# Kernel optimization log

Measured on AMD Instinct MI355X. Metric: run time of the kernel, lower is better.

The kernel has to match this reference:

```python
import jax, jax.numpy as jnp
import numpy as np

TWO_PI = 2.0 * np.pi
LN_EPS = 1e-5


def _periods(out_dim, nb):
    # periods[i,j,g] = i*(out_dim*nb) + j*nb + g + 2
    return jnp.arange(out_dim * out_dim * nb, dtype=jnp.float32).reshape(out_dim, out_dim, nb) + 2.0


def _layer(x, M, gamma, beta, P, residual):
    # x: (B,S,in), M: (out,in), P: (out,out,nb)
    out_dim, _, nb = P.shape
    S = x.shape[1]
    xt = jnp.matmul(x, M.T)  # (B,S,out)
    mu = jnp.mean(xt, axis=-1, keepdims=True)
    var = jnp.mean((xt - mu) ** 2, axis=-1, keepdims=True)
    xn = (xt - mu) / jnp.sqrt(var + LN_EPS) * gamma + beta
    pos = jnp.arange(S, dtype=jnp.float32)[:, None, None, None]  # (S,1,1,1)
    phi = jnp.cos(TWO_PI * pos / _periods(out_dim, nb)[None])  # (S,out,out,nb)
    W = jnp.einsum('ijg,sijg->sij', P, phi)  # (S,out,out) contract basis first
    Nk = jnp.einsum('bsj,sij->bsi', xn, W)  # (B,S,out)
    return Nk + residual


def setup_inputs() -> dict:
    key = jax.random.key(0)
    ks = jax.random.split(key, 8)
    B, S, D_in, D, NB = 8, 1024, 64, 96, 8
    u = lambda k, shape, a: jax.random.uniform(k, shape, jnp.float32, -a, a)
    return {
        'seq': jax.random.normal(ks[0], (B, S, D_in), jnp.float32),
        'M1': u(ks[1], (D, D_in), 0.5),
        'P1': u(ks[2], (D, D, NB), 0.1),
        'Wres1': u(ks[3], (D, D_in), 0.1),
        'g1': jnp.ones((D,), jnp.float32),
        'b1': jnp.zeros((D,), jnp.float32),
        'M2': u(ks[4], (D, D), 0.5),
        'P2': u(ks[5], (D, D, NB), 0.1),
        'g2': jnp.ones((D,), jnp.float32),
        'b2': jnp.zeros((D,), jnp.float32),
    }


def reference(seq, M1, P1, Wres1, g1, b1, M2, P2, g2, b2):
    # Layer 1: 64 -> 96, 'separate' residual uses a Linear projection
    x1 = _layer(seq, M1, g1, b1, P1, jnp.matmul(seq, Wres1.T))
    # Layer 2: 96 -> 96, 'separate' residual with in_dim==out_dim is Identity
    x2 = _layer(x1, M2, g2, b2, P2, x1)
    return x2
```

## Files before the change

kernel.cpp:

```cpp
#include <hip/hip_runtime.h>
#include <hip/hip_fp16.h>

#define S_LEN    1024
#define B_SZ     8
#define D_IN     64
#define D_OUT    96
#define NB       8
#define NE       (D_OUT * D_OUT)
#define CHUNK    16
#define NCHUNK   (S_LEN / CHUNK)
#define NT_W     256
#define NWBLK    (NCHUNK * (NE / NT_W))
#define NT_C     512
#define HPAD     104
#define SPAD     100
#define XPAD     68

__device__ __forceinline__ float cos_rev(float v) {
    v -= floorf(v);
    return __builtin_amdgcn_cosf(v);
}

__global__ void __launch_bounds__(NT_W)
w_kernel(const float* __restrict__ P1, const float* __restrict__ P2,
         __half* __restrict__ W1, __half* __restrict__ W2) {
    const int c  = blockIdx.x / (NE / NT_W);
    const int eb = blockIdx.x % (NE / NT_W);
    const int e  = eb * NT_W + threadIdx.x;
    const int s0 = c * CHUNK;
    const float s0f = (float)s0;

    float p1l[NB], p2l[NB];
    *(float4*)&p1l[0] = *(const float4*)(P1 + e * NB);
    *(float4*)&p1l[4] = *(const float4*)(P1 + e * NB + 4);
    *(float4*)&p2l[0] = *(const float4*)(P2 + e * NB);
    *(float4*)&p2l[4] = *(const float4*)(P2 + e * NB + 4);

    float cc[NB], cp[NB], kk[NB];
    #pragma unroll
    for (int g = 0; g < NB; ++g) {
        const float inv = __builtin_amdgcn_rcpf((float)(e * NB + 2 + g));
        cc[g] = cos_rev(s0f * inv);
        cp[g] = cos_rev((s0f - 1.0f) * inv);
        kk[g] = 2.0f * __builtin_amdgcn_cosf(inv);
    }

    #pragma unroll 4
    for (int s = s0; s < s0 + CHUNK; ++s) {
        float a1 = 0.0f, a2 = 0.0f;
        #pragma unroll
        for (int g = 0; g < NB; ++g) {
            a1 = fmaf(p1l[g], cc[g], a1);
            a2 = fmaf(p2l[g], cc[g], a2);
        }
        W1[s * NE + e] = __float2half(a1);
        W2[s * NE + e] = __float2half(a2);
        #pragma unroll
        for (int g = 0; g < NB; ++g) {
            float cn = fmaf(kk[g], cc[g], -cp[g]);
            cp[g] = cc[g];
            cc[g] = cn;
        }
    }
}

__device__ __forceinline__ float nkdot(const __half* __restrict__ wrow,
                                       const float* __restrict__ xr) {
    float acc = 0.0f;
    #pragma unroll
    for (int h = 0; h < 2; ++h) {
        #pragma unroll
        for (int j = h * 6; j < h * 6 + 6; ++j) {
            float4 raw = *(const float4*)(wrow + 8 * j);
            const __half2* hp = (const __half2*)&raw;
            float2 c0 = __half22float2(hp[0]);
            float2 c1 = __half22float2(hp[1]);
            float2 c2 = __half22float2(hp[2]);
            float2 c3 = __half22float2(hp[3]);
            float4 x0 = *(const float4*)(xr + 8 * j);
            float4 x1 = *(const float4*)(xr + 8 * j + 4);
            acc = fmaf(c0.x, x0.x, acc); acc = fmaf(c0.y, x0.y, acc);
            acc = fmaf(c1.x, x0.z, acc); acc = fmaf(c1.y, x0.w, acc);
            acc = fmaf(c2.x, x1.x, acc); acc = fmaf(c2.y, x1.y, acc);
            acc = fmaf(c3.x, x1.z, acc); acc = fmaf(c3.y, x1.w, acc);
        }
    }
    return acc;
}

__device__ __forceinline__ void stage_W(__half* __restrict__ wh,
                                        const __half* __restrict__ Wg,
                                        int tid) {
    for (int cidx = tid; cidx < NE / 8; cidx += NT_C) {
        const int i = cidx / 12;
        const int j = (cidx % 12) * 8;
        *(float4*)(wh + i * HPAD + j) = *(const float4*)(Wg + cidx * 8);
    }
}

__global__ void __launch_bounds__(NT_C)
consumer(const float* __restrict__ seq,
         const float* __restrict__ M1, const float* __restrict__ Wres1,
         const float* __restrict__ M2,
         const float* __restrict__ g1, const float* __restrict__ b1,
         const float* __restrict__ g2, const float* __restrict__ b2,
         const __half* __restrict__ W1g, const __half* __restrict__ W2g,
         float* __restrict__ out) {
    __shared__ __align__(16) __half wh [D_OUT * HPAD];
    __shared__ __align__(16) float  xn [B_SZ * SPAD];
    __shared__ __align__(16) float  x1b[B_SZ * SPAD];

    const int s   = blockIdx.x;
    const int tid = threadIdx.x;

    stage_W(wh, W1g + (size_t)s * NE, tid);
    {
        int b = tid >> 6, k = tid & 63;
        x1b[b * SPAD + k] = seq[((size_t)b * S_LEN + s) * D_IN + k];
    }
    __syncthreads();

    float ar0 = 0.0f, ar1 = 0.0f;
    for (int pass = 0; pass < 2; ++pass) {
        int idx = tid + pass * NT_C;
        if (idx >= B_SZ * D_OUT) break;
        int i = idx >> 3, b = idx & 7;
        const float4* m  = (const float4*)(M1 + i * D_IN);
        const float4* wr = (const float4*)(Wres1 + i * D_IN);
        const float*  xr = x1b + b * SPAD;
        float at = 0.0f, ar = 0.0f;
        #pragma unroll
        for (int k = 0; k < D_IN / 4; ++k) {
            float4 mv = m[k], rv = wr[k];
            float x0 = xr[4*k], x1 = xr[4*k+1], x2 = xr[4*k+2], x3 = xr[4*k+3];
            at = fmaf(mv.x, x0, fmaf(mv.y, x1, fmaf(mv.z, x2, fmaf(mv.w, x3, at))));
            ar = fmaf(rv.x, x0, fmaf(rv.y, x1, fmaf(rv.z, x2, fmaf(rv.w, x3, ar))));
        }
        xn[b * SPAD + i] = at;
        if (pass == 0) ar0 = ar; else ar1 = ar;
    }
    __syncthreads();

    {
        const int b = tid >> 6, lane = tid & 63;
        const bool lo = (lane < 32);
        float* row = xn + b * SPAD;
        float v0 = row[lane];
        float v1 = lo ? row[64 + lane] : 0.0f;
        float sum = v0 + v1, sq = fmaf(v0, v0, v1 * v1);
        #pragma unroll
        for (int off = 32; off > 0; off >>= 1) {
            sum += __shfl_down(sum, off, 64);
            sq  += __shfl_down(sq,  off, 64);
        }
        sum = __shfl(sum, 0, 64);
        sq  = __shfl(sq,  0, 64);
        const float mu  = sum * (1.0f / 96.0f);
        const float var = fmaf(sq, 1.0f / 96.0f, -(mu * mu));
        const float rs  = rsqrtf(var + 1e-5f);
        row[lane] = fmaf((v0 - mu) * rs, g1[lane], b1[lane]);
        if (lo) row[64 + lane] = fmaf((v1 - mu) * rs, g1[64 + lane], b1[64 + lane]);
    }
    __syncthreads();

    for (int pass = 0; pass < 2; ++pass) {
        int idx = tid + pass * NT_C;
        if (idx >= B_SZ * D_OUT) break;
        int i = idx >> 3, b = idx & 7;
        float ar = (pass == 0) ? ar0 : ar1;
        x1b[b * SPAD + i] = ar + nkdot(wh + i * HPAD, xn + b * SPAD);
    }
    __syncthreads();

    stage_W(wh, W2g + (size_t)s * NE, tid);

    for (int pass = 0; pass < 2; ++pass) {
        int idx = tid + pass * NT_C;
        if (idx >= B_SZ * D_OUT) break;
        int i = idx >> 3, b = idx & 7;
        const float4* m  = (const float4*)(M2 + i * D_OUT);
        const float*  xr = x1b + b * SPAD;
        float at = 0.0f;
        #pragma unroll
        for (int k = 0; k < D_OUT / 4; ++k) {
            float4 mv = m[k];
            at = fmaf(mv.x, xr[4*k], fmaf(mv.y, xr[4*k+1],
                 fmaf(mv.z, xr[4*k+2], fmaf(mv.w, xr[4*k+3], at))));
        }
        xn[b * SPAD + i] = at;
    }
    __syncthreads();

    {
        const int b = tid >> 6, lane = tid & 63;
        const bool lo = (lane < 32);
        float* row = xn + b * SPAD;
        float v0 = row[lane];
        float v1 = lo ? row[64 + lane] : 0.0f;
        float sum = v0 + v1, sq = fmaf(v0, v0, v1 * v1);
        #pragma unroll
        for (int off = 32; off > 0; off >>= 1) {
            sum += __shfl_down(sum, off, 64);
            sq  += __shfl_down(sq,  off, 64);
        }
        sum = __shfl(sum, 0, 64);
        sq  = __shfl(sq,  0, 64);
        const float mu  = sum * (1.0f / 96.0f);
        const float var = fmaf(sq, 1.0f / 96.0f, -(mu * mu));
        const float rs  = rsqrtf(var + 1e-5f);
        row[lane] = fmaf((v0 - mu) * rs, g2[lane], b2[lane]);
        if (lo) row[64 + lane] = fmaf((v1 - mu) * rs, g2[64 + lane], b2[64 + lane]);
    }
    __syncthreads();

    for (int pass = 0; pass < 2; ++pass) {
        int idx = tid + pass * NT_C;
        if (idx >= B_SZ * D_OUT) break;
        int i = idx >> 3, b = idx & 7;
        float acc = nkdot(wh + i * HPAD, xn + b * SPAD);
        out[((size_t)b * S_LEN + s) * D_OUT + i] = acc + x1b[b * SPAD + i];
    }
}

__global__ void __launch_bounds__(NT_W)
hier_fallback(const float* __restrict__ seq,  const float* __restrict__ M1,
              const float* __restrict__ P1,   const float* __restrict__ Wres1,
              const float* __restrict__ g1,   const float* __restrict__ b1,
              const float* __restrict__ M2,   const float* __restrict__ P2,
              const float* __restrict__ g2,   const float* __restrict__ b2,
              float* __restrict__ out) {
    __shared__ __align__(16) float w[D_OUT * SPAD];
    __shared__ __align__(16) float xin[B_SZ * XPAD];
    __shared__ __align__(16) float xn [B_SZ * SPAD];
    __shared__ __align__(16) float x1b[B_SZ * SPAD];
    const int s = blockIdx.x, tid = threadIdx.x;
    const float sf = (float)s;

    for (int idx = tid; idx < B_SZ * D_IN; idx += NT_W) {
        int b = idx >> 6, k = idx & (D_IN - 1);
        xin[b * XPAD + k] = seq[(b * S_LEN + s) * D_IN + k];
    }
    for (int e = tid; e < NE; e += NT_W) {
        float pl[8];
        *(float4*)&pl[0] = *(const float4*)(P1 + e * NB);
        *(float4*)&pl[4] = *(const float4*)(P1 + e * NB + 4);
        float acc = 0.0f;
        #pragma unroll
        for (int g = 0; g < NB; ++g) {
            float v = sf * __builtin_amdgcn_rcpf((float)(e * NB + 2 + g));
            acc = fmaf(pl[g], cos_rev(v), acc);
        }
        int i = e / D_OUT;
        w[e + (SPAD - D_OUT) * i] = acc;
    }
    __syncthreads();
    for (int idx = tid; idx < B_SZ * D_OUT; idx += NT_W) {
        int i = idx >> 3, b = idx & 7;
        const float4* m  = (const float4*)(M1 + i * D_IN);
        const float4* wr = (const float4*)(Wres1 + i * D_IN);
        const float*  xr = xin + b * XPAD;
        float at = 0.0f, ar = 0.0f;
        #pragma unroll
        for (int k = 0; k < D_IN / 4; ++k) {
            float4 mv = m[k], rv = wr[k];
            float x0 = xr[4*k], x1 = xr[4*k+1], x2 = xr[4*k+2], x3 = xr[4*k+3];
            at = fmaf(mv.x, x0, fmaf(mv.y, x1, fmaf(mv.z, x2, fmaf(mv.w, x3, at))));
            ar = fmaf(rv.x, x0, fmaf(rv.y, x1, fmaf(rv.z, x2, fmaf(rv.w, x3, ar))));
        }
        xn [b * SPAD + i] = at;
        x1b[b * SPAD + i] = ar;
    }
    __syncthreads();
    {
        const int b = tid >> 5, rr = tid & 31;
        float* row = xn + b * SPAD;
        float v0 = row[rr], v1 = row[rr + 32], v2 = row[rr + 64];
        float sum = v0 + v1 + v2, sq = fmaf(v0, v0, fmaf(v1, v1, v2 * v2));
        #pragma unroll
        for (int off = 16; off > 0; off >>= 1) {
            sum += __shfl_down(sum, off, 32);
            sq  += __shfl_down(sq,  off, 32);
        }
        sum = __shfl(sum, 0, 32); sq = __shfl(sq, 0, 32);
        float mu = sum * (1.0f/96.0f), var = fmaf(sq, 1.0f/96.0f, -(mu*mu));
        float rs = rsqrtf(var + 1e-5f);
        row[rr]      = fmaf((v0 - mu) * rs, g1[rr],      b1[rr]);
        row[rr + 32] = fmaf((v1 - mu) * rs, g1[rr + 32], b1[rr + 32]);
        row[rr + 64] = fmaf((v2 - mu) * rs, g1[rr + 64], b1[rr + 64]);
    }
    __syncthreads();
    for (int idx = tid; idx < B_SZ * D_OUT; idx += NT_W) {
        int i = idx >> 3, b = idx & 7;
        const float* wrow = w + i * SPAD;
        const float* xr   = xn + b * SPAD;
        float acc = 0.0f;
        #pragma unroll
        for (int j = 0; j < D_OUT / 4; ++j) {
            float4 wv = *(const float4*)(wrow + 4 * j);
            float4 xv = *(const float4*)(xr + 4 * j);
            acc = fmaf(wv.x, xv.x, fmaf(wv.y, xv.y, fmaf(wv.z, xv.z, fmaf(wv.w, xv.w, acc))));
        }
        x1b[b * SPAD + i] += acc;
    }
    __syncthreads();
    for (int e = tid; e < NE; e += NT_W) {
        float pl[8];
        *(float4*)&pl[0] = *(const float4*)(P2 + e * NB);
        *(float4*)&pl[4] = *(const float4*)(P2 + e * NB + 4);
        float acc = 0.0f;
        #pragma unroll
        for (int g = 0; g < NB; ++g) {
            float v = sf * __builtin_amdgcn_rcpf((float)(e * NB + 2 + g));
            acc = fmaf(pl[g], cos_rev(v), acc);
        }
        int i = e / D_OUT;
        w[e + (SPAD - D_OUT) * i] = acc;
    }
    for (int idx = tid; idx < B_SZ * D_OUT; idx += NT_W) {
        int i = idx >> 3, b = idx & 7;
        const float4* m  = (const float4*)(M2 + i * D_OUT);
        const float*  xr = x1b + b * SPAD;
        float at = 0.0f;
        #pragma unroll
        for (int k = 0; k < D_OUT / 4; ++k) {
            float4 mv = m[k];
            at = fmaf(mv.x, xr[4*k], fmaf(mv.y, xr[4*k+1],
                 fmaf(mv.z, xr[4*k+2], fmaf(mv.w, xr[4*k+3], at))));
        }
        xn[b * SPAD + i] = at;
    }
    __syncthreads();
    {
        const int b = tid >> 5, rr = tid & 31;
        float* row = xn + b * SPAD;
        float v0 = row[rr], v1 = row[rr + 32], v2 = row[rr + 64];
        float sum = v0 + v1 + v2, sq = fmaf(v0, v0, fmaf(v1, v1, v2 * v2));
        #pragma unroll
        for (int off = 16; off > 0; off >>= 1) {
            sum += __shfl_down(sum, off, 32);
            sq  += __shfl_down(sq,  off, 32);
        }
        sum = __shfl(sum, 0, 32); sq = __shfl(sq, 0, 32);
        float mu = sum * (1.0f/96.0f), var = fmaf(sq, 1.0f/96.0f, -(mu*mu));
        float rs = rsqrtf(var + 1e-5f);
        row[rr]      = fmaf((v0 - mu) * rs, g2[rr],      b2[rr]);
        row[rr + 32] = fmaf((v1 - mu) * rs, g2[rr + 32], b2[rr + 32]);
        row[rr + 64] = fmaf((v2 - mu) * rs, g2[rr + 64], b2[rr + 64]);
    }
    __syncthreads();
    for (int idx = tid; idx < B_SZ * D_OUT; idx += NT_W) {
        int i = idx >> 3, b = idx & 7;
        const float* wrow = w + i * SPAD;
        const float* xr   = xn + b * SPAD;
        float acc = 0.0f;
        #pragma unroll
        for (int j = 0; j < D_OUT / 4; ++j) {
            float4 wv = *(const float4*)(wrow + 4 * j);
            float4 xv = *(const float4*)(xr + 4 * j);
            acc = fmaf(wv.x, xv.x, fmaf(wv.y, xv.y, fmaf(wv.z, xv.z, fmaf(wv.w, xv.w, acc))));
        }
        out[(b * S_LEN + s) * D_OUT + i] = acc + x1b[b * SPAD + i];
    }
}

extern "C" void kernel_launch(void* const* d_in, const int* in_sizes, int n_in,
                              void* d_out, int out_size, void* d_ws, size_t ws_size,
                              hipStream_t stream) {
    const float* seq   = (const float*)d_in[0];
    const float* M1    = (const float*)d_in[1];
    const float* P1    = (const float*)d_in[2];
    const float* Wres1 = (const float*)d_in[3];
    const float* g1    = (const float*)d_in[4];
    const float* b1    = (const float*)d_in[5];
    const float* M2    = (const float*)d_in[6];
    const float* P2    = (const float*)d_in[7];
    const float* g2    = (const float*)d_in[8];
    const float* b2    = (const float*)d_in[9];
    float* out = (float*)d_out;

    const size_t need = (size_t)2 * S_LEN * NE * sizeof(__half);
    if (ws_size >= need) {
        __half* W1 = (__half*)d_ws;
        __half* W2 = W1 + (size_t)S_LEN * NE;
        w_kernel<<<dim3(NWBLK), dim3(NT_W), 0, stream>>>(P1, P2, W1, W2);
        consumer<<<dim3(S_LEN), dim3(NT_C), 0, stream>>>(
            seq, M1, Wres1, M2, g1, b1, g2, b2, W1, W2, out);
    } else {
        hier_fallback<<<dim3(S_LEN), dim3(NT_W), 0, stream>>>(
            seq, M1, P1, Wres1, g1, b1, M2, P2, g2, b2, out);
    }
}
```

Before: 120.4 us.

## Fuse projection matmul with LayerNorm per wavefront and enlarge W chunk size

The consumer kernel now gives each wavefront one batch row. It computes the input projection and residual for that row directly in registers and reduces mean and variance with shuffles, so the intermediate shared-memory round trip and one barrier per layer go away. The residual is stored into x1b and the Nk dot product is accumulated into it in place. The W-generation chunk size is doubled, which halves the number of w_kernel blocks and changes per-block work. Projection work is now uneven, with half the lanes doing two rows, and M1/M2 rows are read with a lane-strided pattern that may coalesce less well.

```diff
diff --git a/kernel.cpp b/kernel.cpp
--- a/kernel.cpp
+++ b/kernel.cpp
@@ -7,7 +7,7 @@
 #define D_OUT    96
 #define NB       8
 #define NE       (D_OUT * D_OUT)
-#define CHUNK    16
+#define CHUNK    32
 #define NCHUNK   (S_LEN / CHUNK)
 #define NT_W     256
 #define NWBLK    (NCHUNK * (NE / NT_W))
@@ -110,44 +110,47 @@
     __shared__ __align__(16) float  xn [B_SZ * SPAD];
     __shared__ __align__(16) float  x1b[B_SZ * SPAD];
 
-    const int s   = blockIdx.x;
-    const int tid = threadIdx.x;
+    const int s    = blockIdx.x;
+    const int tid  = threadIdx.x;
+    const int wv   = tid >> 6;
+    const int lane = tid & 63;
+
+    {
+        x1b[wv * SPAD + lane] = seq[((size_t)wv * S_LEN + s) * D_IN + lane];
+    }
+    __syncthreads();
 
     stage_W(wh, W1g + (size_t)s * NE, tid);
+
     {
-        int b = tid >> 6, k = tid & 63;
-        x1b[b * SPAD + k] = seq[((size_t)b * S_LEN + s) * D_IN + k];
-    }
-    __syncthreads();
-
-    float ar0 = 0.0f, ar1 = 0.0f;
-    for (int pass = 0; pass < 2; ++pass) {
-        int idx = tid + pass * NT_C;
-        if (idx >= B_SZ * D_OUT) break;
-        int i = idx >> 3, b = idx & 7;
-        const float4* m  = (const float4*)(M1 + i * D_IN);
-        const float4* wr = (const float4*)(Wres1 + i * D_IN);
-        const float*  xr = x1b + b * SPAD;
-        float at = 0.0f, ar = 0.0f;
-        #pragma unroll
-        for (int k = 0; k < D_IN / 4; ++k) {
-            float4 mv = m[k], rv = wr[k];
-            float x0 = xr[4*k], x1 = xr[4*k+1], x2 = xr[4*k+2], x3 = xr[4*k+3];
-            at = fmaf(mv.x, x0, fmaf(mv.y, x1, fmaf(mv.z, x2, fmaf(mv.w, x3, at))));
-            ar = fmaf(rv.x, x0, fmaf(rv.y, x1, fmaf(rv.z, x2, fmaf(rv.w, x3, ar))));
-        }
-        xn[b * SPAD + i] = at;
-        if (pass == 0) ar0 = ar; else ar1 = ar;
-    }
-    __syncthreads();
-
-    {
-        const int b = tid >> 6, lane = tid & 63;
+        const int b = wv;
+        const float* xr = x1b + b * SPAD;
         const bool lo = (lane < 32);
-        float* row = xn + b * SPAD;
-        float v0 = row[lane];
-        float v1 = lo ? row[64 + lane] : 0.0f;
-        float sum = v0 + v1, sq = fmaf(v0, v0, v1 * v1);
+        float xt0 = 0.0f, rs0 = 0.0f, xt1 = 0.0f, rs1 = 0.0f;
+        {
+            const float4* m0 = (const float4*)(M1 + lane * D_IN);
+            const float4* r0 = (const float4*)(Wres1 + lane * D_IN);
+            #pragma unroll
+            for (int k = 0; k < D_IN / 4; ++k) {
+                float4 mv = m0[k], rv = r0[k];
+                float x0 = xr[4*k], x1 = xr[4*k+1], x2 = xr[4*k+2], x3 = xr[4*k+3];
+                xt0 = fmaf(mv.x, x0, fmaf(mv.y, x1, fmaf(mv.z, x2, fmaf(mv.w, x3, xt0))));
+                rs0 = fmaf(rv.x, x0, fmaf(rv.y, x1, fmaf(rv.z, x2, fmaf(rv.w, x3, rs0))));
+            }
+        }
+        if (lo) {
+            const float4* m1 = (const float4*)(M1 + (lane + 64) * D_IN);
+            const float4* r1 = (const float4*)(Wres1 + (lane + 64) * D_IN);
+            #pragma unroll
+            for (int k = 0; k < D_IN / 4; ++k) {
+                float4 mv = m1[k], rv = r1[k];
+                float x0 = xr[4*k], x1 = xr[4*k+1], x2 = xr[4*k+2], x3 = xr[4*k+3];
+                xt1 = fmaf(mv.x, x0, fmaf(mv.y, x1, fmaf(mv.z, x2, fmaf(mv.w, x3, xt1))));
+                rs1 = fmaf(rv.x, x0, fmaf(rv.y, x1, fmaf(rv.z, x2, fmaf(rv.w, x3, rs1))));
+            }
+        }
+        float sum = xt0 + xt1;
+        float sq  = fmaf(xt0, xt0, xt1 * xt1);
         #pragma unroll
         for (int off = 32; off > 0; off >>= 1) {
             sum += __shfl_down(sum, off, 64);
@@ -157,47 +160,52 @@
         sq  = __shfl(sq,  0, 64);
         const float mu  = sum * (1.0f / 96.0f);
         const float var = fmaf(sq, 1.0f / 96.0f, -(mu * mu));
-        const float rs  = rsqrtf(var + 1e-5f);
-        row[lane] = fmaf((v0 - mu) * rs, g1[lane], b1[lane]);
-        if (lo) row[64 + lane] = fmaf((v1 - mu) * rs, g1[64 + lane], b1[64 + lane]);
+        const float rsc = rsqrtf(var + 1e-5f);
+        xn [b * SPAD + lane] = fmaf((xt0 - mu) * rsc, g1[lane], b1[lane]);
+        x1b[b * SPAD + lane] = rs0;
+        if (lo) {
+            xn [b * SPAD + 64 + lane] = fmaf((xt1 - mu) * rsc, g1[64 + lane], b1[64 + lane]);
+            x1b[b * SPAD + 64 + lane] = rs1;
+        }
     }
     __syncthreads();
 
     for (int pass = 0; pass < 2; ++pass) {
         int idx = tid + pass * NT_C;
-        if (idx >= B_SZ * D_OUT) break;
-        int i = idx >> 3, b = idx & 7;
-        float ar = (pass == 0) ? ar0 : ar1;
-        x1b[b * SPAD + i] = ar + nkdot(wh + i * HPAD, xn + b * SPAD);
+        if (idx < B_SZ * D_OUT) {
+            int i = idx >> 3, b = idx & 7;
+            x1b[b * SPAD + i] += nkdot(wh + i * HPAD, xn + b * SPAD);
+        }
     }
     __syncthreads();
 
     stage_W(wh, W2g + (size_t)s * NE, tid);
 
-    for (int pass = 0; pass < 2; ++pass) {
-        int idx = tid + pass * NT_C;
-        if (idx >= B_SZ * D_OUT) break;
-        int i = idx >> 3, b = idx & 7;
-        const float4* m  = (const float4*)(M2 + i * D_OUT);
-        const float*  xr = x1b + b * SPAD;
-        float at = 0.0f;
-        #pragma unroll
-        for (int k = 0; k < D_OUT / 4; ++k) {
-            float4 mv = m[k];
-            at = fmaf(mv.x, xr[4*k], fmaf(mv.y, xr[4*k+1],
-                 fmaf(mv.z, xr[4*k+2], fmaf(mv.w, xr[4*k+3], at))));
-        }
-        xn[b * SPAD + i] = at;
-    }
-    __syncthreads();
-
     {
-        const int b = tid >> 6, lane = tid & 63;
+        const int b = wv;
+        const float* xr = x1b + b * SPAD;
         const bool lo = (lane < 32);
-        float* row = xn + b * SPAD;
-        float v0 = row[lane];
-        float v1 = lo ? row[64 + lane] : 0.0f;
-        float sum = v0 + v1, sq = fmaf(v0, v0, v1 * v1);
+        float xt0 = 0.0f, xt1 = 0.0f;
+        {
+            const float4* m0 = (const float4*)(M2 + lane * D_OUT);
+            #pragma unroll
+            for (int k = 0; k < D_OUT / 4; ++k) {
+                float4 mv = m0[k];
+                xt0 = fmaf(mv.x, xr[4*k], fmaf(mv.y, xr[4*k+1],
+                      fmaf(mv.z, xr[4*k+2], fmaf(mv.w, xr[4*k+3], xt0))));
+            }
+        }
+        if (lo) {
+            const float4* m1 = (const float4*)(M2 + (lane + 64) * D_OUT);
+            #pragma unroll
+            for (int k = 0; k < D_OUT / 4; ++k) {
+                float4 mv = m1[k];
+                xt1 = fmaf(mv.x, xr[4*k], fmaf(mv.y, xr[4*k+1],
+                      fmaf(mv.z, xr[4*k+2], fmaf(mv.w, xr[4*k+3], xt1))));
+            }
+        }
+        float sum = xt0 + xt1;
+        float sq  = fmaf(xt0, xt0, xt1 * xt1);
         #pragma unroll
         for (int off = 32; off > 0; off >>= 1) {
             sum += __shfl_down(sum, off, 64);
@@ -207,18 +215,20 @@
         sq  = __shfl(sq,  0, 64);
         const float mu  = sum * (1.0f / 96.0f);
         const float var = fmaf(sq, 1.0f / 96.0f, -(mu * mu));
-        const float rs  = rsqrtf(var + 1e-5f);
-        row[lane] = fmaf((v0 - mu) * rs, g2[lane], b2[lane]);
-        if (lo) row[64 + lane] = fmaf((v1 - mu) * rs, g2[64 + lane], b2[64 + lane]);
+        const float rsc = rsqrtf(var + 1e-5f);
+        xn[b * SPAD + lane] = fmaf((xt0 - mu) * rsc, g2[lane], b2[lane]);
+        if (lo)
+            xn[b * SPAD + 64 + lane] = fmaf((xt1 - mu) * rsc, g2[64 + lane], b2[64 + lane]);
     }
     __syncthreads();
 
     for (int pass = 0; pass < 2; ++pass) {
         int idx = tid + pass * NT_C;
-        if (idx >= B_SZ * D_OUT) break;
-        int i = idx >> 3, b = idx & 7;
-        float acc = nkdot(wh + i * HPAD, xn + b * SPAD);
-        out[((size_t)b * S_LEN + s) * D_OUT + i] = acc + x1b[b * SPAD + i];
+        if (idx < B_SZ * D_OUT) {
+            int i = idx >> 3, b = idx & 7;
+            float acc = nkdot(wh + i * HPAD, xn + b * SPAD);
+            out[((size_t)b * S_LEN + s) * D_OUT + i] = acc + x1b[b * SPAD + i];
+        }
     }
 }
 
```

Result: slower. 192.6 us (+60.0%).
